# Kernel tuning notes

Hardware: AMD Instinct MI355X
Metric: run time of the kernel (lower is better)

The kernel has to match this reference:

```python
import jax, jax.numpy as jnp
import numpy as np
import math

D_MODEL = 512
NUM_HEADS = 8
B, L = 2, 4096
EPS_NORM = 1e-8
PLASTICITY = 1.0


def setup_inputs() -> dict:
    key = jax.random.key(0)
    ks = jax.random.split(key, 6)
    D, H = D_MODEL, NUM_HEADS
    std = 1.0 / math.sqrt(D)
    x = jax.random.normal(ks[0], (B, L, D), dtype=jnp.float32)
    qkv_w = jax.random.normal(ks[1], (3 * D, D), dtype=jnp.float32) * std
    qkv_b = jnp.zeros((3 * D,), dtype=jnp.float32)
    out_w = jax.random.normal(ks[2], (D, D), dtype=jnp.float32) * std
    out_b = jnp.zeros((D,), dtype=jnp.float32)
    decay_w = jax.random.normal(ks[3], (H, D), dtype=jnp.float32) * 0.02
    decay_b = jnp.full((H,), 4.0, dtype=jnp.float32)
    norm_scale = jnp.ones((D,), dtype=jnp.float32)
    return {"x": x, "qkv_w": qkv_w, "qkv_b": qkv_b, "out_w": out_w,
            "out_b": out_b, "decay_w": decay_w, "decay_b": decay_b,
            "norm_scale": norm_scale}


def _hebbian_forward(x, qkv_w, qkv_b, out_w, out_b, decay_w, decay_b, norm_scale):
    Bsz, Lsz, D = x.shape
    H = NUM_HEADS
    E = D // H
    # QKV projection (torch Linear: y = x @ W.T + b)
    qkv = x @ qkv_w.T + qkv_b
    q, k, v = jnp.split(qkv, 3, axis=-1)
    q = q.reshape(Bsz, Lsz, H, E)
    k = k.reshape(Bsz, Lsz, H, E)
    v = v.reshape(Bsz, Lsz, H, E)
    # feature map: elu(x) + 1
    q = (jax.nn.elu(q) + 1.0) / math.sqrt(E)
    k = jax.nn.elu(k) + 1.0
    # input-dependent decay per head
    decay_logits = x @ decay_w.T + decay_b          # (B,L,H)
    lambdas = (0.9 + 0.1 * jax.nn.sigmoid(decay_logits)) * PLASTICITY
    log_lambdas = jnp.log(jnp.clip(lambdas, 1e-6))[..., None]   # (B,L,H,1)
    log_lambda_cum = jnp.clip(jnp.cumsum(log_lambdas, axis=1), -50.0, 50.0)
    decay_k = jnp.exp(-log_lambda_cum)
    decay_q = jnp.exp(log_lambda_cum)
    k_decayed = k * decay_k
    q_decayed = q * decay_q
    # outer-product memory state cumsum: (B,L,H,E,E)
    kv = jnp.einsum('blhe,blhf->blhef', k_decayed, v)
    memory_state = jnp.cumsum(kv, axis=1)
    k_sum_decayed = jnp.cumsum(k_decayed, axis=1)
    num = jnp.einsum('blhe,blhef->blhf', q_decayed, memory_state)
    den = jnp.einsum('blhe,blhe->blh', q_decayed, k_sum_decayed)[..., None] + 1e-6
    out = (num / den).reshape(Bsz, Lsz, D)
    out = out @ out_w.T + out_b
    # RMSNorm (dropout is identity in eval)
    rnorm = jax.lax.rsqrt(jnp.mean(out * out, axis=-1, keepdims=True) + EPS_NORM)
    return out * rnorm * norm_scale


def reference(x, qkv_w, qkv_b, out_w, out_b, decay_w, decay_b, norm_scale):
    return _hebbian_forward(x, qkv_w, qkv_b, out_w, out_b, decay_w, decay_b, norm_scale)
```

## Files before the change

kernel.cpp:

```cpp
#include <hip/hip_runtime.h>

typedef unsigned short u16;
typedef unsigned int u32;

#define B_ 2
#define L_ 4096
#define D_ 512
#define H_ 8
#define E_ 64
#define M_ (B_*L_)
#define TD (3*D_)
#define NCH (L_/64)
#define BH (B_*H_)

typedef short bf16x8 __attribute__((ext_vector_type(8)));
typedef float f32x4 __attribute__((ext_vector_type(4)));

__device__ __forceinline__ float bf2f(u16 u){ return __uint_as_float(((u32)u)<<16); }
__device__ __forceinline__ u16 f2bf(float f){
  u32 u = __float_as_uint(f);
  u32 r = u + 0x7FFFu + ((u>>16)&1u);
  return (u16)(r>>16);
}
__device__ __forceinline__ float elu1(float v){ return v>0.f ? v+1.f : expf(v); }

__device__ __forceinline__ void async_ld16(const u16* g, u16* l){
  __builtin_amdgcn_global_load_lds(
      (const __attribute__((address_space(1))) void*)g,
      (__attribute__((address_space(3))) void*)l, 16, 0, 0);
}

__global__ __launch_bounds__(256) void decay_conv_kernel(const float* __restrict__ x,
    const float* __restrict__ dw, const float* __restrict__ db,
    const float* __restrict__ qw, const float* __restrict__ ow,
    float* __restrict__ ll, u16* __restrict__ xb,
    u16* __restrict__ qwb, u16* __restrict__ owb)
{
  int blk = blockIdx.x;
  if (blk < 2048){
    int wv = threadIdx.x>>6, lane = threadIdx.x&63;
    int m = blk*4 + wv;
    float xr[8];
    #pragma unroll
    for (int i=0;i<8;i++) xr[i] = x[(size_t)m*D_ + lane + 64*i];
    #pragma unroll
    for (int i=0;i<8;i++) xb[(size_t)m*D_ + lane + 64*i] = f2bf(xr[i]);
    int b = m >> 12, l = m & (L_-1);
    for (int h=0; h<H_; h++){
      float acc = 0.f;
      #pragma unroll
      for (int i=0;i<8;i++) acc += xr[i]*dw[h*D_ + lane + 64*i];
      #pragma unroll
      for (int off=32; off>0; off>>=1) acc += __shfl_xor(acc, off);
      if (lane == h){
        float z = acc + db[h];
        float lam = 0.9f + 0.1f/(1.f + expf(-z));
        ll[((b*H_+h)*L_) + l] = logf(lam);
      }
    }
  } else {
    int gid = (blk-2048)*256 + threadIdx.x;
    const float* src; u16* dst; int off;
    if (gid < 196608){ src = qw; dst = qwb; off = gid; }
    else { src = ow; dst = owb; off = gid - 196608; }
    float4 v = ((const float4*)src)[off];
    ushort4 o; o.x=f2bf(v.x); o.y=f2bf(v.y); o.z=f2bf(v.z); o.w=f2bf(v.w);
    ((ushort4*)dst)[off] = o;
  }
}

__global__ __launch_bounds__(256) void scan_kernel(const float* __restrict__ ll,
    float* __restrict__ cb)
{
  int bh = blockIdx.x, t = threadIdx.x;
  int lane = t & 63, wv = t >> 6;
  const float* p = ll + (size_t)bh*L_ + t*16;
  float s[16];
  #pragma unroll
  for (int q=0;q<4;q++){
    float4 v = *(const float4*)(p + q*4);
    s[q*4+0]=v.x; s[q*4+1]=v.y; s[q*4+2]=v.z; s[q*4+3]=v.w;
  }
  #pragma unroll
  for (int i=1;i<16;i++) s[i] += s[i-1];
  float tot = s[15];
  float ws = tot;
  #pragma unroll
  for (int off=1; off<64; off<<=1){
    float tmp = __shfl_up(ws, off);
    if (lane >= off) ws += tmp;
  }
  __shared__ float wsum[4];
  if (lane == 63) wsum[wv] = ws;
  __syncthreads();
  float base = 0.f;
  #pragma unroll
  for (int w2=0; w2<3; w2++) if (w2 < wv) base += wsum[w2];
  float ex = base + ws - tot;
  float* c = cb + (size_t)bh*L_ + t*16;
  #pragma unroll
  for (int i=0;i<16;i++) c[i] = fminf(50.f, fmaxf(-50.f, ex + s[i]));
}

template<bool OB>
__global__ __launch_bounds__(256) void gemm_mfma(const u16* __restrict__ A,
    const u16* __restrict__ W, const float* __restrict__ bias,
    void* __restrict__ Cv, int M, int N, int K)
{
  __shared__ u16 As[128*32];
  __shared__ u16 Bs[128*32];
  int n0 = blockIdx.x*128, m0 = blockIdx.y*128;
  int t = threadIdx.x, wave = t>>6, lane = t&63;
  int wm = (wave>>1)*64, wn = (wave&1)*64;
  f32x4 acc[4][4] = {};
  int srow = wave*32 + (lane>>2);
  int scol = (lane&3)*8;
  const u16* gA = A + (size_t)(m0+srow)*K + scol;
  const u16* gB = W + (size_t)(n0+srow)*K + scol;
  u16* lA = As + wave*1024;
  u16* lB = Bs + wave*1024;
  int q8 = (lane>>4)*8, r16 = lane&15;
  for (int k0=0; k0<K; k0+=32){
    async_ld16(gA + k0,                lA);
    async_ld16(gA + k0 + 16*(size_t)K, lA + 512);
    async_ld16(gB + k0,                lB);
    async_ld16(gB + k0 + 16*(size_t)K, lB + 512);
    __syncthreads();
    bf16x8 af[4], bfr[4];
    #pragma unroll
    for (int i=0;i<4;i++) af[i]  = *(const bf16x8*)&As[(wm + i*16 + r16)*32 + q8];
    #pragma unroll
    for (int j=0;j<4;j++) bfr[j] = *(const bf16x8*)&Bs[(wn + j*16 + r16)*32 + q8];
    #pragma unroll
    for (int i=0;i<4;i++)
      #pragma unroll
      for (int j=0;j<4;j++)
        acc[i][j] = __builtin_amdgcn_mfma_f32_16x16x32_bf16(af[i], bfr[j], acc[i][j], 0,0,0);
    __syncthreads();
  }
  #pragma unroll
  for (int i=0;i<4;i++){
    int row = m0 + wm + i*16 + (lane>>4)*4;
    #pragma unroll
    for (int j=0;j<4;j++){
      int col = n0 + wn + j*16 + r16;
      float bv = bias[col];
      #pragma unroll
      for (int r=0;r<4;r++){
        float val = acc[i][j][r] + bv;
        if (OB) ((u16*)Cv)[(size_t)(row+r)*N + col] = f2bf(val);
        else    ((float*)Cv)[(size_t)(row+r)*N + col] = val;
      }
    }
  }
}

__global__ __launch_bounds__(256) void transform_sums_kernel(const u16* __restrict__ qkvb,
    const float* __restrict__ cb, u16* __restrict__ qc, u16* __restrict__ kc,
    u16* __restrict__ vtc, u16* __restrict__ Stc, float* __restrict__ ksc)
{
  int bid = blockIdx.x;
  int bh = bid >> 6, ch = bid & 63;
  int b = bh >> 3, h = bh & 7;
  __shared__ u16 Ks[64*68];
  __shared__ u16 Vs[64*68];
  __shared__ u16 Ktl[4096];
  __shared__ u16 Vtl[4096];
  __shared__ float ksr[256];
  int t = threadIdx.x;
  size_t mbase = (size_t)b*L_ + ch*64;
  #pragma unroll
  for (int i=0;i<2;i++){
    int idx = t + 256*i;
    int l = idx>>3, e0 = (idx&7)*8;
    int kh = e0>>5, ej = e0&31;
    float c = cb[(size_t)bh*L_ + ch*64 + l];
    float eqc = expf(c)*0.125f, ekc = expf(-c);
    const u16* src = qkvb + (mbase+l)*TD + h*64 + e0;
    u16 in[8], o[8];
    *(ushort4*)&in[0] = *(const ushort4*)(src);
    *(ushort4*)&in[4] = *(const ushort4*)(src+4);
    #pragma unroll
    for (int j=0;j<8;j++) o[j] = f2bf(elu1(bf2f(in[j]))*eqc);
    u16* qd = qc + ((size_t)bid*2 + kh)*2048 + l*32 + ej;
    *(ushort4*)qd = *(ushort4*)&o[0];
    *(ushort4*)(qd+4) = *(ushort4*)&o[4];
    *(ushort4*)&in[0] = *(const ushort4*)(src + D_);
    *(ushort4*)&in[4] = *(const ushort4*)(src + D_ + 4);
    #pragma unroll
    for (int j=0;j<8;j++) o[j] = f2bf(elu1(bf2f(in[j]))*ekc);
    u16* kd = kc + ((size_t)bid*2 + kh)*2048 + l*32 + ej;
    *(ushort4*)kd = *(ushort4*)&o[0];
    *(ushort4*)(kd+4) = *(ushort4*)&o[4];
    *(ushort4*)&Ks[l*68+e0]   = *(ushort4*)&o[0];
    *(ushort4*)&Ks[l*68+e0+4] = *(ushort4*)&o[4];
    *(ushort4*)&Vs[l*68+e0]   = *(const ushort4*)(src + 2*D_);
    *(ushort4*)&Vs[l*68+e0+4] = *(const ushort4*)(src + 2*D_ + 4);
  }
  __syncthreads();
  int e = t & 63, jq = t >> 6;
  {
    u16 kv[16], vv[16];
    float ksum = 0.f;
    #pragma unroll
    for (int jj=0;jj<16;jj++){
      int j = jq*16+jj;
      kv[jj] = Ks[j*68 + e];
      ksum += bf2f(kv[jj]);
      vv[jj] = Vs[j*68 + e];
    }
    int kh = jq>>1, jl = (jq&1)*16;
    u16* kt = &Ktl[(kh*64 + e)*32 + jl];
    u16* vt = &Vtl[(kh*64 + e)*32 + jl];
    #pragma unroll
    for (int s=0;s<4;s++){
      *(ushort4*)(kt + s*4) = *(ushort4*)&kv[s*4];
      *(ushort4*)(vt + s*4) = *(ushort4*)&vv[s*4];
    }
    ksr[t] = ksum;
  }
  __syncthreads();
  {
    *(uint4*)&vtc[(size_t)bid*4096 + t*8]        = *(const uint4*)&Vtl[t*8];
    *(uint4*)&vtc[(size_t)bid*4096 + 2048 + t*8] = *(const uint4*)&Vtl[2048 + t*8];
  }
  int w = t>>6, lane = t&63;
  int r16 = lane & 15, q8 = (lane>>4)*8;
  bf16x8 av[2];
  #pragma unroll
  for (int kh=0;kh<2;kh++)
    av[kh] = *(const bf16x8*)&Vtl[(kh*64 + w*16 + r16)*32 + q8];
  f32x4 acc[4] = {};
  #pragma unroll
  for (int et=0;et<4;et++)
    #pragma unroll
    for (int kh=0;kh<2;kh++){
      bf16x8 bv = *(const bf16x8*)&Ktl[(kh*64 + et*16 + r16)*32 + q8];
      acc[et] = __builtin_amdgcn_mfma_f32_16x16x32_bf16(av[kh], bv, acc[et], 0,0,0);
    }
  #pragma unroll
  for (int et=0;et<4;et++){
    int eh = et>>1, el = (et&1)*16 + r16;
    #pragma unroll
    for (int r=0;r<4;r++){
      int f = w*16 + (lane>>4)*4 + r;
      Stc[((size_t)bid*2 + eh)*2048 + f*32 + el] = f2bf(acc[et][r]);
    }
  }
  if (t < 64) ksc[bid*64 + t] = ksr[t] + ksr[64+t] + ksr[128+t] + ksr[192+t];
}

__global__ __launch_bounds__(256) void chunk_prefix_kernel(u16* __restrict__ Stc,
    float* __restrict__ ksc)
{
  int gid = blockIdx.x*256 + threadIdx.x;
  int bh = gid >> 11, e2 = gid & 2047;
  u32* p = (u32*)Stc + (size_t)bh*131072 + e2;
  float r0 = 0.f, r1 = 0.f;
  #pragma unroll 4
  for (int ch=0; ch<NCH; ch++){
    u32 v = p[ch*2048];
    float lo = bf2f((u16)(v & 0xffffu));
    float hi = bf2f((u16)(v >> 16));
    p[ch*2048] = (u32)f2bf(r0) | ((u32)f2bf(r1) << 16);
    r0 += lo; r1 += hi;
  }
  if (gid < BH*64){
    int bh2 = gid >> 6, e = gid & 63;
    float* kp = ksc + bh2*4096 + e;
    float kr = 0.f;
    #pragma unroll 4
    for (int ch=0; ch<NCH; ch++){
      float v = kp[ch*64]; kp[ch*64] = kr; kr += v;
    }
  }
}

__global__ __launch_bounds__(256) void chunk_out_kernel(const u16* __restrict__ qc,
    const u16* __restrict__ kc, const u16* __restrict__ vtc,
    const u16* __restrict__ Stc, const float* __restrict__ ksc,
    u16* __restrict__ attn)
{
  int bid = blockIdx.x;
  int bh = bid >> 6, ch = bid & 63;
  int b = bh >> 3, h = bh & 7;
  __shared__ u16 KV[16384];
  __shared__ u16 Ab[4096];
  __shared__ float kp[64], den4[256], den[64];
  int t = threadIdx.x, w = t>>6, lane = t&63;
  size_t mbase = (size_t)b*L_ + ch*64;
  const u16* srcs[4] = { qc, kc, vtc, Stc };
  {
    const u16* gbase = srcs[w] + (size_t)bid*4096 + lane*8;
    #pragma unroll
    for (int q=0;q<8;q++)
      async_ld16(gbase + q*512, KV + w*4096 + q*512);
  }
  if (t < 64) kp[t] = ksc[bid*64 + t];
  __syncthreads();
  const u16* Qs   = KV;
  const u16* Kb_s = KV + 4096;
  const u16* Vt_s = KV + 8192;
  const u16* St_s = KV + 12288;
  int r16 = lane & 15, q8 = (lane>>4)*8;
  bf16x8 aq[2];
  #pragma unroll
  for (int eh=0;eh<2;eh++)
    aq[eh] = *(const bf16x8*)&Qs[(eh*64 + w*16 + r16)*32 + q8];
  f32x4 accA[4] = {};
  #pragma unroll
  for (int jt=0;jt<4;jt++)
    #pragma unroll
    for (int eh=0;eh<2;eh++){
      bf16x8 bv = *(const bf16x8*)&Kb_s[(eh*64 + jt*16 + r16)*32 + q8];
      accA[jt] = __builtin_amdgcn_mfma_f32_16x16x32_bf16(aq[eh], bv, accA[jt], 0,0,0);
    }
  int l4 = t>>2, q4 = t&3;
  float dkp = 0.f;
  {
    int eh = q4>>1, el0 = (q4&1)*16;
    bf16x8 x1 = *(const bf16x8*)&Qs[(eh*64 + l4)*32 + el0];
    bf16x8 x2 = *(const bf16x8*)&Qs[(eh*64 + l4)*32 + el0 + 8];
    #pragma unroll
    for (int i=0;i<8;i++)
      dkp += bf2f((u16)x1[i])*kp[q4*16+i] + bf2f((u16)x2[i])*kp[q4*16+8+i];
  }
  #pragma unroll
  for (int jt=0;jt<4;jt++)
    #pragma unroll
    for (int r=0;r<4;r++){
      int lr = w*16 + ((lane>>4)<<2) + r;
      int j  = jt*16 + r16;
      Ab[((jt>>1)*64 + lr)*32 + (jt&1)*16 + r16] = (j <= lr) ? f2bf(accA[jt][r]) : (u16)0;
    }
  __syncthreads();
  float dA = 0.f;
  {
    int jh2 = q4>>1, jl0 = (q4&1)*16;
    bf16x8 y1 = *(const bf16x8*)&Ab[(jh2*64 + l4)*32 + jl0];
    bf16x8 y2 = *(const bf16x8*)&Ab[(jh2*64 + l4)*32 + jl0 + 8];
    #pragma unroll
    for (int i=0;i<8;i++) dA += bf2f((u16)y1[i]) + bf2f((u16)y2[i]);
  }
  den4[t] = dkp + dA;
  __syncthreads();
  if (t < 64) den[t] = den4[t*4] + den4[t*4+1] + den4[t*4+2] + den4[t*4+3] + 1e-6f;
  bf16x8 aA[2];
  #pragma unroll
  for (int jh=0;jh<2;jh++)
    aA[jh] = *(const bf16x8*)&Ab[(jh*64 + w*16 + r16)*32 + q8];
  f32x4 acc[4] = {};
  #pragma unroll
  for (int ft=0;ft<4;ft++){
    #pragma unroll
    for (int jh=0;jh<2;jh++){
      bf16x8 bv = *(const bf16x8*)&Vt_s[(jh*64 + ft*16 + r16)*32 + q8];
      acc[ft] = __builtin_amdgcn_mfma_f32_16x16x32_bf16(aA[jh], bv, acc[ft], 0,0,0);
    }
    #pragma unroll
    for (int eh=0;eh<2;eh++){
      bf16x8 bv = *(const bf16x8*)&St_s[(eh*64 + ft*16 + r16)*32 + q8];
      acc[ft] = __builtin_amdgcn_mfma_f32_16x16x32_bf16(aq[eh], bv, acc[ft], 0,0,0);
    }
  }
  __syncthreads();
  float inv[4];
  #pragma unroll
  for (int r=0;r<4;r++) inv[r] = 1.f / den[w*16 + ((lane>>4)<<2) + r];
  #pragma unroll
  for (int ft=0;ft<4;ft++)
    #pragma unroll
    for (int r=0;r<4;r++){
      int lr = w*16 + ((lane>>4)<<2) + r;
      attn[(mbase + lr)*D_ + h*64 + ft*16 + r16] = f2bf(acc[ft][r]*inv[r]);
    }
}

__global__ __launch_bounds__(256) void rmsnorm_kernel(const u16* __restrict__ mid,
    const float* __restrict__ scale, float* __restrict__ out)
{
  int m = blockIdx.x, t = threadIdx.x;
  const u16* row = mid + (size_t)m*D_;
  float v0 = bf2f(row[t]), v1 = bf2f(row[t+256]);
  float ss = v0*v0 + v1*v1;
  #pragma unroll
  for (int off=32; off>0; off>>=1) ss += __shfl_xor(ss, off);
  __shared__ float red[4];
  if ((t&63)==0) red[t>>6] = ss;
  __syncthreads();
  float tot = red[0]+red[1]+red[2]+red[3];
  float r = rsqrtf(tot*(1.f/512.f) + 1e-8f);
  out[(size_t)m*D_ + t]       = v0*r*scale[t];
  out[(size_t)m*D_ + t + 256] = v1*r*scale[t+256];
}

extern "C" void kernel_launch(void* const* d_in, const int* in_sizes, int n_in,
                              void* d_out, int out_size, void* d_ws, size_t ws_size,
                              hipStream_t stream)
{
  const float* x     = (const float*)d_in[0];
  const float* w_qkv = (const float*)d_in[1];
  const float* b_qkv = (const float*)d_in[2];
  const float* w_out = (const float*)d_in[3];
  const float* b_out = (const float*)d_in[4];
  const float* w_dec = (const float*)d_in[5];
  const float* b_dec = (const float*)d_in[6];
  const float* gnorm = (const float*)d_in[7];
  float* out = (float*)d_out;

  char* ws = (char*)d_ws;
  u16*   qkvb = (u16*)(ws);
  u16*   qc   = (u16*)(ws + 25165824);
  u16*   kc   = (u16*)(ws + 33554432);
  u16*   vtc  = (u16*)(ws + 41943040);
  u16*   Stc  = (u16*)(ws + 50331648);
  float* ksc  = (float*)(ws + 58720256);
  float* ll   = (float*)(ws + 58982400);
  float* cb   = (float*)(ws + 59244544);
  u16*   xb   = (u16*)(ws + 59506688);
  u16*   qwb  = (u16*)(ws + 67895296);
  u16*   owb  = (u16*)(ws + 69468160);
  u16*   midb = qkvb;
  u16*   attn = xb;

  decay_conv_kernel<<<dim3(3072), dim3(256), 0, stream>>>(x, w_dec, b_dec, w_qkv, w_out,
                                                          ll, xb, qwb, owb);
  scan_kernel<<<dim3(BH), dim3(256), 0, stream>>>(ll, cb);
  gemm_mfma<true><<<dim3(TD/128, M_/128), dim3(256), 0, stream>>>(xb, qwb, b_qkv, qkvb, M_, TD, D_);
  transform_sums_kernel<<<dim3(BH*NCH), dim3(256), 0, stream>>>(qkvb, cb, qc, kc, vtc, Stc, ksc);
  chunk_prefix_kernel<<<dim3(128), dim3(256), 0, stream>>>(Stc, ksc);
  chunk_out_kernel<<<dim3(BH*NCH), dim3(256), 0, stream>>>(qc, kc, vtc, Stc, ksc, attn);
  gemm_mfma<true><<<dim3(D_/128, M_/128), dim3(256), 0, stream>>>(attn, owb, b_out, midb, M_, D_, D_);
  rmsnorm_kernel<<<dim3(M_), dim3(256), 0, stream>>>(midb, gnorm, out);
}
```

Baseline: 172.0 us.

## Fuse QKV projection GEMM into per-chunk transform kernel

Replaces the standalone QKV GEMM plus transform_sums kernel with a single kernel in which each (batch, head, chunk) block computes its 64x192 slice of Q/K/V directly with MFMA. It then applies the elu/decay scaling, writes the chunk layouts, and computes the per-chunk K^T V state and K sums in place. This removes the round trip of the full bf16 QKV intermediate through global memory and one launch. In exchange, the GEMM tile is smaller (64x192 per block, 4x3 MFMA tiles per wave), which gives less operand reuse, and the x tile is reloaded once per head across 8 heads.

```diff
diff --git a/kernel.cpp b/kernel.cpp
--- a/kernel.cpp
+++ b/kernel.cpp
@@ -102,10 +102,273 @@
   for (int i=0;i<16;i++) c[i] = fminf(50.f, fmaxf(-50.f, ex + s[i]));
 }
 
-template<bool OB>
+__global__ __launch_bounds__(256) void qkv_chunk_kernel(
+    const u16* __restrict__ xb, const u16* __restrict__ qwb,
+    const float* __restrict__ b_qkv, const float* __restrict__ cb,
+    u16* __restrict__ qc, u16* __restrict__ kc, u16* __restrict__ vtc,
+    u16* __restrict__ Stc, float* __restrict__ ksc)
+{
+  int bid = blockIdx.x;
+  int bh = bid >> 6, ch = bid & 63;
+  int b = bh >> 3, h = bh & 7;
+  __shared__ u16 pool[8192];
+  __shared__ u16 Qs[64*68], Ks[64*68], Vs[64*68];
+  __shared__ float eqcl[64], ekcl[64], ksr[256];
+  int t = threadIdx.x, w = t>>6, lane = t&63;
+  int r16 = lane&15, q4 = lane>>4, q8 = q4*8;
+  size_t mbase = (size_t)b*L_ + ch*64;
+  if (t < 64){
+    float c = cb[(size_t)bh*L_ + ch*64 + t];
+    eqcl[t] = 0.125f*expf(c);
+    ekcl[t] = expf(-c);
+  }
+  const u16* gsrc[4];
+  #pragma unroll
+  for (int q=0;q<4;q++){
+    int ci = w*4 + q;
+    int row = ci*16 + (lane>>2);
+    int kl = (lane&3)*8;
+    if (ci < 4){
+      gsrc[q] = xb + (mbase + row)*(size_t)D_ + kl;
+    } else {
+      int wrow = row - 64;
+      int sec = wrow >> 6, e = wrow & 63;
+      gsrc[q] = qwb + (size_t)(sec*D_ + h*64 + e)*D_ + kl;
+    }
+  }
+  f32x4 acc[4][3] = {};
+  for (int k0=0; k0<D_; k0+=32){
+    #pragma unroll
+    for (int q=0;q<4;q++)
+      async_ld16(gsrc[q] + k0, pool + (w*4+q)*512);
+    __syncthreads();
+    bf16x8 af[4], bf[3];
+    #pragma unroll
+    for (int i=0;i<4;i++) af[i] = *(const bf16x8*)&pool[(i*16 + r16)*32 + q8];
+    #pragma unroll
+    for (int j=0;j<3;j++) bf[j] = *(const bf16x8*)&pool[2048 + (w*48 + j*16 + r16)*32 + q8];
+    #pragma unroll
+    for (int i=0;i<4;i++)
+      #pragma unroll
+      for (int j=0;j<3;j++)
+        acc[i][j] = __builtin_amdgcn_mfma_f32_16x16x32_bf16(af[i], bf[j], acc[i][j], 0,0,0);
+    __syncthreads();
+  }
+  #pragma unroll
+  for (int j=0;j<3;j++){
+    int ncol = w*48 + j*16 + r16;
+    int sec = ncol >> 6, e = ncol & 63;
+    float bv = b_qkv[sec*D_ + h*64 + e];
+    u16* dst = (sec==0) ? Qs : (sec==1) ? Ks : Vs;
+    #pragma unroll
+    for (int i=0;i<4;i++)
+      #pragma unroll
+      for (int r=0;r<4;r++){
+        int l = i*16 + q4*4 + r;
+        float val = acc[i][j][r] + bv;
+        float o;
+        if (sec==0)      o = elu1(val)*eqcl[l];
+        else if (sec==1) o = elu1(val)*ekcl[l];
+        else             o = val;
+        dst[l*68 + e] = f2bf(o);
+      }
+  }
+  __syncthreads();
+  #pragma unroll
+  for (int i=0;i<2;i++){
+    int idx = t + 256*i;
+    int l = idx>>3, e0 = (idx&7)*8;
+    int kh = e0>>5, ej = e0&31;
+    ushort4 a0 = *(const ushort4*)&Qs[l*68+e0];
+    ushort4 a1 = *(const ushort4*)&Qs[l*68+e0+4];
+    u16* qd = qc + ((size_t)bid*2 + kh)*2048 + l*32 + ej;
+    *(ushort4*)qd = a0; *(ushort4*)(qd+4) = a1;
+    ushort4 b0 = *(const ushort4*)&Ks[l*68+e0];
+    ushort4 b1 = *(const ushort4*)&Ks[l*68+e0+4];
+    u16* kd = kc + ((size_t)bid*2 + kh)*2048 + l*32 + ej;
+    *(ushort4*)kd = b0; *(ushort4*)(kd+4) = b1;
+  }
+  u16* Ktl = pool;
+  u16* Vtl = pool + 4096;
+  {
+    int e = t & 63, jq = t >> 6;
+    u16 kv[16], vv[16];
+    float ksum = 0.f;
+    #pragma unroll
+    for (int jj=0;jj<16;jj++){
+      int j = jq*16+jj;
+      kv[jj] = Ks[j*68 + e];
+      ksum += bf2f(kv[jj]);
+      vv[jj] = Vs[j*68 + e];
+    }
+    int kh = jq>>1, jl = (jq&1)*16;
+    u16* kt = &Ktl[(kh*64 + e)*32 + jl];
+    u16* vt = &Vtl[(kh*64 + e)*32 + jl];
+    #pragma unroll
+    for (int s=0;s<4;s++){
+      *(ushort4*)(kt + s*4) = *(ushort4*)&kv[s*4];
+      *(ushort4*)(vt + s*4) = *(ushort4*)&vv[s*4];
+    }
+    ksr[t] = ksum;
+  }
+  __syncthreads();
+  *(uint4*)&vtc[(size_t)bid*4096 + t*8]        = *(const uint4*)&Vtl[t*8];
+  *(uint4*)&vtc[(size_t)bid*4096 + 2048 + t*8] = *(const uint4*)&Vtl[2048 + t*8];
+  {
+    bf16x8 av[2];
+    #pragma unroll
+    for (int kh=0;kh<2;kh++)
+      av[kh] = *(const bf16x8*)&Vtl[(kh*64 + w*16 + r16)*32 + q8];
+    f32x4 sacc[4] = {};
+    #pragma unroll
+    for (int et=0;et<4;et++)
+      #pragma unroll
+      for (int kh=0;kh<2;kh++){
+        bf16x8 bv = *(const bf16x8*)&Ktl[(kh*64 + et*16 + r16)*32 + q8];
+        sacc[et] = __builtin_amdgcn_mfma_f32_16x16x32_bf16(av[kh], bv, sacc[et], 0,0,0);
+      }
+    #pragma unroll
+    for (int et=0;et<4;et++){
+      int eh = et>>1, el = (et&1)*16 + r16;
+      #pragma unroll
+      for (int r=0;r<4;r++){
+        int f = w*16 + q4*4 + r;
+        Stc[((size_t)bid*2 + eh)*2048 + f*32 + el] = f2bf(sacc[et][r]);
+      }
+    }
+  }
+  if (t < 64) ksc[bid*64 + t] = ksr[t] + ksr[64+t] + ksr[128+t] + ksr[192+t];
+}
+
+__global__ __launch_bounds__(256) void chunk_prefix_kernel(u16* __restrict__ Stc,
+    float* __restrict__ ksc)
+{
+  int gid = blockIdx.x*256 + threadIdx.x;
+  int bh = gid >> 11, e2 = gid & 2047;
+  u32* p = (u32*)Stc + (size_t)bh*131072 + e2;
+  float r0 = 0.f, r1 = 0.f;
+  #pragma unroll 4
+  for (int ch=0; ch<NCH; ch++){
+    u32 v = p[ch*2048];
+    float lo = bf2f((u16)(v & 0xffffu));
+    float hi = bf2f((u16)(v >> 16));
+    p[ch*2048] = (u32)f2bf(r0) | ((u32)f2bf(r1) << 16);
+    r0 += lo; r1 += hi;
+  }
+  if (gid < BH*64){
+    int bh2 = gid >> 6, e = gid & 63;
+    float* kp = ksc + bh2*4096 + e;
+    float kr = 0.f;
+    #pragma unroll 4
+    for (int ch=0; ch<NCH; ch++){
+      float v = kp[ch*64]; kp[ch*64] = kr; kr += v;
+    }
+  }
+}
+
+__global__ __launch_bounds__(256) void chunk_out_kernel(const u16* __restrict__ qc,
+    const u16* __restrict__ kc, const u16* __restrict__ vtc,
+    const u16* __restrict__ Stc, const float* __restrict__ ksc,
+    u16* __restrict__ attn)
+{
+  int bid = blockIdx.x;
+  int bh = bid >> 6, ch = bid & 63;
+  int b = bh >> 3, h = bh & 7;
+  __shared__ u16 KV[16384];
+  __shared__ u16 Ab[4096];
+  __shared__ float kp[64], den4[256], den[64];
+  int t = threadIdx.x, w = t>>6, lane = t&63;
+  size_t mbase = (size_t)b*L_ + ch*64;
+  const u16* srcs[4] = { qc, kc, vtc, Stc };
+  {
+    const u16* gbase = srcs[w] + (size_t)bid*4096 + lane*8;
+    #pragma unroll
+    for (int q=0;q<8;q++)
+      async_ld16(gbase + q*512, KV + w*4096 + q*512);
+  }
+  if (t < 64) kp[t] = ksc[bid*64 + t];
+  __syncthreads();
+  const u16* Qs   = KV;
+  const u16* Kb_s = KV + 4096;
+  const u16* Vt_s = KV + 8192;
+  const u16* St_s = KV + 12288;
+  int r16 = lane & 15, q8 = (lane>>4)*8;
+  bf16x8 aq[2];
+  #pragma unroll
+  for (int eh=0;eh<2;eh++)
+    aq[eh] = *(const bf16x8*)&Qs[(eh*64 + w*16 + r16)*32 + q8];
+  f32x4 accA[4] = {};
+  #pragma unroll
+  for (int jt=0;jt<4;jt++)
+    #pragma unroll
+    for (int eh=0;eh<2;eh++){
+      bf16x8 bv = *(const bf16x8*)&Kb_s[(eh*64 + jt*16 + r16)*32 + q8];
+      accA[jt] = __builtin_amdgcn_mfma_f32_16x16x32_bf16(aq[eh], bv, accA[jt], 0,0,0);
+    }
+  int l4 = t>>2, q4 = t&3;
+  float dkp = 0.f;
+  {
+    int eh = q4>>1, el0 = (q4&1)*16;
+    bf16x8 x1 = *(const bf16x8*)&Qs[(eh*64 + l4)*32 + el0];
+    bf16x8 x2 = *(const bf16x8*)&Qs[(eh*64 + l4)*32 + el0 + 8];
+    #pragma unroll
+    for (int i=0;i<8;i++)
+      dkp += bf2f((u16)x1[i])*kp[q4*16+i] + bf2f((u16)x2[i])*kp[q4*16+8+i];
+  }
+  #pragma unroll
+  for (int jt=0;jt<4;jt++)
+    #pragma unroll
+    for (int r=0;r<4;r++){
+      int lr = w*16 + ((lane>>4)<<2) + r;
+      int j  = jt*16 + r16;
+      Ab[((jt>>1)*64 + lr)*32 + (jt&1)*16 + r16] = (j <= lr) ? f2bf(accA[jt][r]) : (u16)0;
+    }
+  __syncthreads();
+  float dA = 0.f;
+  {
+    int jh2 = q4>>1, jl0 = (q4&1)*16;
+    bf16x8 y1 = *(const bf16x8*)&Ab[(jh2*64 + l4)*32 + jl0];
+    bf16x8 y2 = *(const bf16x8*)&Ab[(jh2*64 + l4)*32 + jl0 + 8];
+    #pragma unroll
+    for (int i=0;i<8;i++) dA += bf2f((u16)y1[i]) + bf2f((u16)y2[i]);
+  }
+  den4[t] = dkp + dA;
+  __syncthreads();
+  if (t < 64) den[t] = den4[t*4] + den4[t*4+1] + den4[t*4+2] + den4[t*4+3] + 1e-6f;
+  bf16x8 aA[2];
+  #pragma unroll
+  for (int jh=0;jh<2;jh++)
+    aA[jh] = *(const bf16x8*)&Ab[(jh*64 + w*16 + r16)*32 + q8];
+  f32x4 acc[4] = {};
+  #pragma unroll
+  for (int ft=0;ft<4;ft++){
+    #pragma unroll
+    for (int jh=0;jh<2;jh++){
+      bf16x8 bv = *(const bf16x8*)&Vt_s[(jh*64 + ft*16 + r16)*32 + q8];
+      acc[ft] = __builtin_amdgcn_mfma_f32_16x16x32_bf16(aA[jh], bv, acc[ft], 0,0,0);
+    }
+    #pragma unroll
+    for (int eh=0;eh<2;eh++){
+      bf16x8 bv = *(const bf16x8*)&St_s[(eh*64 + ft*16 + r16)*32 + q8];
+      acc[ft] = __builtin_amdgcn_mfma_f32_16x16x32_bf16(aq[eh], bv, acc[ft], 0,0,0);
+    }
+  }
+  __syncthreads();
+  float inv[4];
+  #pragma unroll
+  for (int r=0;r<4;r++) inv[r] = 1.f / den[w*16 + ((lane>>4)<<2) + r];
+  #pragma unroll
+  for (int ft=0;ft<4;ft++)
+    #pragma unroll
+    for (int r=0;r<4;r++){
+      int lr = w*16 + ((lane>>4)<<2) + r;
+      attn[(mbase + lr)*D_ + h*64 + ft*16 + r16] = f2bf(acc[ft][r]*inv[r]);
+    }
+}
+
 __global__ __launch_bounds__(256) void gemm_mfma(const u16* __restrict__ A,
     const u16* __restrict__ W, const float* __restrict__ bias,
-    void* __restrict__ Cv, int M, int N, int K)
+    u16* __restrict__ C, int M, int N, int K)
 {
   __shared__ u16 As[128*32];
   __shared__ u16 Bs[128*32];
@@ -146,234 +409,10 @@
       int col = n0 + wn + j*16 + r16;
       float bv = bias[col];
       #pragma unroll
-      for (int r=0;r<4;r++){
-        float val = acc[i][j][r] + bv;
-        if (OB) ((u16*)Cv)[(size_t)(row+r)*N + col] = f2bf(val);
-        else    ((float*)Cv)[(size_t)(row+r)*N + col] = val;
-      }
-    }
-  }
-}
-
-__global__ __launch_bounds__(256) void transform_sums_kernel(const u16* __restrict__ qkvb,
-    const float* __restrict__ cb, u16* __restrict__ qc, u16* __restrict__ kc,
-    u16* __restrict__ vtc, u16* __restrict__ Stc, float* __restrict__ ksc)
-{
-  int bid = blockIdx.x;
-  int bh = bid >> 6, ch = bid & 63;
-  int b = bh >> 3, h = bh & 7;
-  __shared__ u16 Ks[64*68];
-  __shared__ u16 Vs[64*68];
-  __shared__ u16 Ktl[4096];
-  __shared__ u16 Vtl[4096];
-  __shared__ float ksr[256];
-  int t = threadIdx.x;
-  size_t mbase = (size_t)b*L_ + ch*64;
-  #pragma unroll
-  for (int i=0;i<2;i++){
-    int idx = t + 256*i;
-    int l = idx>>3, e0 = (idx&7)*8;
-    int kh = e0>>5, ej = e0&31;
-    float c = cb[(size_t)bh*L_ + ch*64 + l];
-    float eqc = expf(c)*0.125f, ekc = expf(-c);
-    const u16* src = qkvb + (mbase+l)*TD + h*64 + e0;
-    u16 in[8], o[8];
-    *(ushort4*)&in[0] = *(const ushort4*)(src);
-    *(ushort4*)&in[4] = *(const ushort4*)(src+4);
-    #pragma unroll
-    for (int j=0;j<8;j++) o[j] = f2bf(elu1(bf2f(in[j]))*eqc);
-    u16* qd = qc + ((size_t)bid*2 + kh)*2048 + l*32 + ej;
-    *(ushort4*)qd = *(ushort4*)&o[0];
-    *(ushort4*)(qd+4) = *(ushort4*)&o[4];
-    *(ushort4*)&in[0] = *(const ushort4*)(src + D_);
-    *(ushort4*)&in[4] = *(const ushort4*)(src + D_ + 4);
-    #pragma unroll
-    for (int j=0;j<8;j++) o[j] = f2bf(elu1(bf2f(in[j]))*ekc);
-    u16* kd = kc + ((size_t)bid*2 + kh)*2048 + l*32 + ej;
-    *(ushort4*)kd = *(ushort4*)&o[0];
-    *(ushort4*)(kd+4) = *(ushort4*)&o[4];
-    *(ushort4*)&Ks[l*68+e0]   = *(ushort4*)&o[0];
-    *(ushort4*)&Ks[l*68+e0+4] = *(ushort4*)&o[4];
-    *(ushort4*)&Vs[l*68+e0]   = *(const ushort4*)(src + 2*D_);
-    *(ushort4*)&Vs[l*68+e0+4] = *(const ushort4*)(src + 2*D_ + 4);
-  }
-  __syncthreads();
-  int e = t & 63, jq = t >> 6;
-  {
-    u16 kv[16], vv[16];
-    float ksum = 0.f;
-    #pragma unroll
-    for (int jj=0;jj<16;jj++){
-      int j = jq*16+jj;
-      kv[jj] = Ks[j*68 + e];
-      ksum += bf2f(kv[jj]);
-      vv[jj] = Vs[j*68 + e];
-    }
-    int kh = jq>>1, jl = (jq&1)*16;
-    u16* kt = &Ktl[(kh*64 + e)*32 + jl];
-    u16* vt = &Vtl[(kh*64 + e)*32 + jl];
-    #pragma unroll
-    for (int s=0;s<4;s++){
-      *(ushort4*)(kt + s*4) = *(ushort4*)&kv[s*4];
-      *(ushort4*)(vt + s*4) = *(ushort4*)&vv[s*4];
-    }
-    ksr[t] = ksum;
-  }
-  __syncthreads();
-  {
-    *(uint4*)&vtc[(size_t)bid*4096 + t*8]        = *(const uint4*)&Vtl[t*8];
-    *(uint4*)&vtc[(size_t)bid*4096 + 2048 + t*8] = *(const uint4*)&Vtl[2048 + t*8];
-  }
-  int w = t>>6, lane = t&63;
-  int r16 = lane & 15, q8 = (lane>>4)*8;
-  bf16x8 av[2];
-  #pragma unroll
-  for (int kh=0;kh<2;kh++)
-    av[kh] = *(const bf16x8*)&Vtl[(kh*64 + w*16 + r16)*32 + q8];
-  f32x4 acc[4] = {};
-  #pragma unroll
-  for (int et=0;et<4;et++)
-    #pragma unroll
-    for (int kh=0;kh<2;kh++){
-      bf16x8 bv = *(const bf16x8*)&Ktl[(kh*64 + et*16 + r16)*32 + q8];
-      acc[et] = __builtin_amdgcn_mfma_f32_16x16x32_bf16(av[kh], bv, acc[et], 0,0,0);
-    }
-  #pragma unroll
-  for (int et=0;et<4;et++){
-    int eh = et>>1, el = (et&1)*16 + r16;
-    #pragma unroll
-    for (int r=0;r<4;r++){
-      int f = w*16 + (lane>>4)*4 + r;
-      Stc[((size_t)bid*2 + eh)*2048 + f*32 + el] = f2bf(acc[et][r]);
-    }
-  }
-  if (t < 64) ksc[bid*64 + t] = ksr[t] + ksr[64+t] + ksr[128+t] + ksr[192+t];
-}
-
-__global__ __launch_bounds__(256) void chunk_prefix_kernel(u16* __restrict__ Stc,
-    float* __restrict__ ksc)
-{
-  int gid = blockIdx.x*256 + threadIdx.x;
-  int bh = gid >> 11, e2 = gid & 2047;
-  u32* p = (u32*)Stc + (size_t)bh*131072 + e2;
-  float r0 = 0.f, r1 = 0.f;
-  #pragma unroll 4
-  for (int ch=0; ch<NCH; ch++){
-    u32 v = p[ch*2048];
-    float lo = bf2f((u16)(v & 0xffffu));
-    float hi = bf2f((u16)(v >> 16));
-    p[ch*2048] = (u32)f2bf(r0) | ((u32)f2bf(r1) << 16);
-    r0 += lo; r1 += hi;
-  }
-  if (gid < BH*64){
-    int bh2 = gid >> 6, e = gid & 63;
-    float* kp = ksc + bh2*4096 + e;
-    float kr = 0.f;
-    #pragma unroll 4
-    for (int ch=0; ch<NCH; ch++){
-      float v = kp[ch*64]; kp[ch*64] = kr; kr += v;
-    }
-  }
-}
-
-__global__ __launch_bounds__(256) void chunk_out_kernel(const u16* __restrict__ qc,
-    const u16* __restrict__ kc, const u16* __restrict__ vtc,
-    const u16* __restrict__ Stc, const float* __restrict__ ksc,
-    u16* __restrict__ attn)
-{
-  int bid = blockIdx.x;
-  int bh = bid >> 6, ch = bid & 63;
-  int b = bh >> 3, h = bh & 7;
-  __shared__ u16 KV[16384];
-  __shared__ u16 Ab[4096];
-  __shared__ float kp[64], den4[256], den[64];
-  int t = threadIdx.x, w = t>>6, lane = t&63;
-  size_t mbase = (size_t)b*L_ + ch*64;
-  const u16* srcs[4] = { qc, kc, vtc, Stc };
-  {
-    const u16* gbase = srcs[w] + (size_t)bid*4096 + lane*8;
-    #pragma unroll
-    for (int q=0;q<8;q++)
-      async_ld16(gbase + q*512, KV + w*4096 + q*512);
-  }
-  if (t < 64) kp[t] = ksc[bid*64 + t];
-  __syncthreads();
-  const u16* Qs   = KV;
-  const u16* Kb_s = KV + 4096;
-  const u16* Vt_s = KV + 8192;
-  const u16* St_s = KV + 12288;
-  int r16 = lane & 15, q8 = (lane>>4)*8;
-  bf16x8 aq[2];
-  #pragma unroll
-  for (int eh=0;eh<2;eh++)
-    aq[eh] = *(const bf16x8*)&Qs[(eh*64 + w*16 + r16)*32 + q8];
-  f32x4 accA[4] = {};
-  #pragma unroll
-  for (int jt=0;jt<4;jt++)
-    #pragma unroll
-    for (int eh=0;eh<2;eh++){
-      bf16x8 bv = *(const bf16x8*)&Kb_s[(eh*64 + jt*16 + r16)*32 + q8];
-      accA[jt] = __builtin_amdgcn_mfma_f32_16x16x32_bf16(aq[eh], bv, accA[jt], 0,0,0);
-    }
-  int l4 = t>>2, q4 = t&3;
-  float dkp = 0.f;
-  {
-    int eh = q4>>1, el0 = (q4&1)*16;
-    bf16x8 x1 = *(const bf16x8*)&Qs[(eh*64 + l4)*32 + el0];
-    bf16x8 x2 = *(const bf16x8*)&Qs[(eh*64 + l4)*32 + el0 + 8];
-    #pragma unroll
-    for (int i=0;i<8;i++)
-      dkp += bf2f((u16)x1[i])*kp[q4*16+i] + bf2f((u16)x2[i])*kp[q4*16+8+i];
-  }
-  #pragma unroll
-  for (int jt=0;jt<4;jt++)
-    #pragma unroll
-    for (int r=0;r<4;r++){
-      int lr = w*16 + ((lane>>4)<<2) + r;
-      int j  = jt*16 + r16;
-      Ab[((jt>>1)*64 + lr)*32 + (jt&1)*16 + r16] = (j <= lr) ? f2bf(accA[jt][r]) : (u16)0;
-    }
-  __syncthreads();
-  float dA = 0.f;
-  {
-    int jh2 = q4>>1, jl0 = (q4&1)*16;
-    bf16x8 y1 = *(const bf16x8*)&Ab[(jh2*64 + l4)*32 + jl0];
-    bf16x8 y2 = *(const bf16x8*)&Ab[(jh2*64 + l4)*32 + jl0 + 8];
-    #pragma unroll
-    for (int i=0;i<8;i++) dA += bf2f((u16)y1[i]) + bf2f((u16)y2[i]);
-  }
-  den4[t] = dkp + dA;
-  __syncthreads();
-  if (t < 64) den[t] = den4[t*4] + den4[t*4+1] + den4[t*4+2] + den4[t*4+3] + 1e-6f;
-  bf16x8 aA[2];
-  #pragma unroll
-  for (int jh=0;jh<2;jh++)
-    aA[jh] = *(const bf16x8*)&Ab[(jh*64 + w*16 + r16)*32 + q8];
-  f32x4 acc[4] = {};
-  #pragma unroll
-  for (int ft=0;ft<4;ft++){
-    #pragma unroll
-    for (int jh=0;jh<2;jh++){
-      bf16x8 bv = *(const bf16x8*)&Vt_s[(jh*64 + ft*16 + r16)*32 + q8];
-      acc[ft] = __builtin_amdgcn_mfma_f32_16x16x32_bf16(aA[jh], bv, acc[ft], 0,0,0);
-    }
-    #pragma unroll
-    for (int eh=0;eh<2;eh++){
-      bf16x8 bv = *(const bf16x8*)&St_s[(eh*64 + ft*16 + r16)*32 + q8];
-      acc[ft] = __builtin_amdgcn_mfma_f32_16x16x32_bf16(aq[eh], bv, acc[ft], 0,0,0);
-    }
-  }
-  __syncthreads();
-  float inv[4];
-  #pragma unroll
-  for (int r=0;r<4;r++) inv[r] = 1.f / den[w*16 + ((lane>>4)<<2) + r];
-  #pragma unroll
-  for (int ft=0;ft<4;ft++)
-    #pragma unroll
-    for (int r=0;r<4;r++){
-      int lr = w*16 + ((lane>>4)<<2) + r;
-      attn[(mbase + lr)*D_ + h*64 + ft*16 + r16] = f2bf(acc[ft][r]*inv[r]);
-    }
+      for (int r=0;r<4;r++)
+        C[(size_t)(row+r)*N + col] = f2bf(acc[i][j][r] + bv);
+    }
+  }
 }
 
 __global__ __launch_bounds__(256) void rmsnorm_kernel(const u16* __restrict__ mid,
@@ -409,27 +448,26 @@
   float* out = (float*)d_out;
 
   char* ws = (char*)d_ws;
-  u16*   qkvb = (u16*)(ws);
-  u16*   qc   = (u16*)(ws + 25165824);
-  u16*   kc   = (u16*)(ws + 33554432);
-  u16*   vtc  = (u16*)(ws + 41943040);
-  u16*   Stc  = (u16*)(ws + 50331648);
-  float* ksc  = (float*)(ws + 58720256);
-  float* ll   = (float*)(ws + 58982400);
-  float* cb   = (float*)(ws + 59244544);
-  u16*   xb   = (u16*)(ws + 59506688);
-  u16*   qwb  = (u16*)(ws + 67895296);
-  u16*   owb  = (u16*)(ws + 69468160);
-  u16*   midb = qkvb;
+  u16*   qc   = (u16*)(ws);
+  u16*   kc   = (u16*)(ws +  8388608);
+  u16*   vtc  = (u16*)(ws + 16777216);
+  u16*   Stc  = (u16*)(ws + 25165824);
+  float* ksc  = (float*)(ws + 33554432);
+  float* ll   = (float*)(ws + 33816576);
+  float* cb   = (float*)(ws + 34078720);
+  u16*   xb   = (u16*)(ws + 34340864);
+  u16*   qwb  = (u16*)(ws + 42729472);
+  u16*   owb  = (u16*)(ws + 44302336);
   u16*   attn = xb;
+  u16*   midb = qc;
 
   decay_conv_kernel<<<dim3(3072), dim3(256), 0, stream>>>(x, w_dec, b_dec, w_qkv, w_out,
                                                           ll, xb, qwb, owb);
   scan_kernel<<<dim3(BH), dim3(256), 0, stream>>>(ll, cb);
-  gemm_mfma<true><<<dim3(TD/128, M_/128), dim3(256), 0, stream>>>(xb, qwb, b_qkv, qkvb, M_, TD, D_);
-  transform_sums_kernel<<<dim3(BH*NCH), dim3(256), 0, stream>>>(qkvb, cb, qc, kc, vtc, Stc, ksc);
+  qkv_chunk_kernel<<<dim3(BH*NCH), dim3(256), 0, stream>>>(xb, qwb, b_qkv, cb,
+                                                           qc, kc, vtc, Stc, ksc);
   chunk_prefix_kernel<<<dim3(128), dim3(256), 0, stream>>>(Stc, ksc);
   chunk_out_kernel<<<dim3(BH*NCH), dim3(256), 0, stream>>>(qc, kc, vtc, Stc, ksc, attn);
-  gemm_mfma<true><<<dim3(D_/128, M_/128), dim3(256), 0, stream>>>(attn, owb, b_out, midb, M_, D_, D_);
+  gemm_mfma<<<dim3(D_/128, M_/128), dim3(256), 0, stream>>>(attn, owb, b_out, midb, M_, D_, D_);
   rmsnorm_kernel<<<dim3(M_), dim3(256), 0, stream>>>(midb, gnorm, out);
 }
```

New measurement: 176.8 us. 2.8% more time.
